# Performance work log

Measured on AMD Instinct MI355X. Metric: run time of the kernel, lower is better.

The kernel has to match this reference:

```python
import jax, jax.numpy as jnp
import numpy as np

N_EMBD = 512
N_HEAD = 8
HEAD = N_EMBD // N_HEAD
EPS = 1e-5

def layernorm(x, g, b):
    mu = jnp.mean(x, axis=-1, keepdims=True)
    var = jnp.mean(jnp.square(x - mu), axis=-1, keepdims=True)
    return (x - mu) * jax.lax.rsqrt(var + EPS) * g + b

def setup_inputs() -> dict:
    key = jax.random.key(0)
    ks = jax.random.split(key, 12)
    B, T, C, H, D = 32, 512, N_EMBD, N_HEAD, HEAD
    s = lambda fan: 1.0 / np.sqrt(fan)
    return {
        "x": jax.random.normal(ks[0], (B, T, C), jnp.float32),
        "wq": jax.random.normal(ks[1], (H, C, D), jnp.float32) * s(C),
        "wk": jax.random.normal(ks[2], (H, C, D), jnp.float32) * s(C),
        "wv": jax.random.normal(ks[3], (H, C, D), jnp.float32) * s(C),
        "w_proj": jax.random.normal(ks[4], (C, C), jnp.float32) * s(C),
        "b_proj": jnp.zeros((C,), jnp.float32),
        "w1": jax.random.normal(ks[5], (C, 4 * C), jnp.float32) * s(C),
        "b1": jnp.zeros((4 * C,), jnp.float32),
        "w2": jax.random.normal(ks[6], (4 * C, C), jnp.float32) * s(4 * C),
        "b2": jnp.zeros((C,), jnp.float32),
        "ln1_g": jnp.ones((C,), jnp.float32),
        "ln1_b": jnp.zeros((C,), jnp.float32),
        "ln2_g": jnp.ones((C,), jnp.float32),
        "ln2_b": jnp.zeros((C,), jnp.float32),
    }

def reference(x, wq, wk, wv, w_proj, b_proj, w1, b1, w2, b2, ln1_g, ln1_b, ln2_g, ln2_b):
    B, T, C = x.shape
    h = layernorm(x, ln1_g, ln1_b)
    q = jnp.einsum('btc,hcd->bhtd', h, wq)
    k = jnp.einsum('btc,hcd->bhtd', h, wk)
    v = jnp.einsum('btc,hcd->bhtd', h, wv)
    # NB: original scales by n_embd**-0.5 (C), not head_size
    scores = jnp.einsum('bhtd,bhsd->bhts', q, k) * (C ** -0.5)
    causal = jnp.tril(jnp.ones((T, T), bool))
    scores = jnp.where(causal, scores, -jnp.inf)
    attn = jax.nn.softmax(scores, axis=-1)
    o = jnp.einsum('bhts,bhsd->bhtd', attn, v)  # [B,H,T,D]
    o = jnp.transpose(o, (0, 2, 1, 3)).reshape(B, T, C)  # concat heads
    x = x + o @ w_proj + b_proj
    h2 = layernorm(x, ln2_g, ln2_b)
    ffn = jax.nn.relu(h2 @ w1 + b1) @ w2 + b2
    return x + ffn
```

## Files before the change

kernel.cpp:

```cpp
#include <hip/hip_runtime.h>
#include <hip/hip_bf16.h>


#define B_  32
#define T_  512
#define C_  512
#define H_  8
#define D_  64
#define BT  (B_*T_)
#define CF  2048

typedef __hip_bfloat16 bf16;
typedef __attribute__((ext_vector_type(8))) short bf16x8;
typedef __attribute__((ext_vector_type(4))) float f32x4;
typedef __attribute__((ext_vector_type(4))) short short4v;

__device__ __forceinline__ float bf2f(bf16 x) { return __bfloat162float(x); }
__device__ __forceinline__ bf16  f2bf(float x){ return __float2bfloat16(x); }
__device__ __forceinline__ short f2bf_bits(float f){
    bf16 h = __float2bfloat16(f);
    return *reinterpret_cast<short*>(&h);
}
__device__ __forceinline__ float bfbits2f(short s){
    unsigned u = ((unsigned)(unsigned short)s) << 16;
    return __uint_as_float(u);
}

#define AS_G __attribute__((address_space(1)))
#define AS_L __attribute__((address_space(3)))

__global__ __launch_bounds__(256) void transpose_all(const float* __restrict__ wq,
                                                     const float* __restrict__ wk,
                                                     const float* __restrict__ wv,
                                                     const float* __restrict__ wproj,
                                                     const float* __restrict__ w1,
                                                     const float* __restrict__ w2,
                                                     bf16* __restrict__ wt)
{
    const int t = blockIdx.x;
    const float* src; int K, Nn, k0, n0; size_t dstoff;
    if (t < 192) {
        const int which = t / 64, w = t % 64, hh = w >> 3, kt = w & 7;
        src = (which == 0 ? wq : which == 1 ? wk : wv) + (size_t)hh * 512 * 64;
        K = 512; Nn = 64; k0 = kt * 64; n0 = 0;
        dstoff = (size_t)(which * 512 + hh * 64) * 512;
    } else if (t < 256) {
        const int i = t - 192;
        src = wproj; K = 512; Nn = 512; n0 = (i & 7) * 64; k0 = (i >> 3) * 64;
        dstoff = (size_t)1536 * 512;
    } else if (t < 512) {
        const int i = t - 256;
        src = w1; K = 512; Nn = 2048; n0 = (i & 31) * 64; k0 = (i >> 5) * 64;
        dstoff = (size_t)2048 * 512;
    } else {
        const int i = t - 512;
        src = w2; K = 2048; Nn = 512; n0 = (i & 7) * 64; k0 = (i >> 3) * 64;
        dstoff = (size_t)2048 * 512 + (size_t)2048 * 512;
    }

    __shared__ float tl[64][65];
    const int tid = threadIdx.x;
    #pragma unroll
    for (int j = 0; j < 16; ++j) {
        const int e = j * 256 + tid, r = e >> 6, c = e & 63;
        tl[r][c] = src[(size_t)(k0 + r) * Nn + n0 + c];
    }
    __syncthreads();
    #pragma unroll
    for (int j = 0; j < 16; ++j) {
        const int e = j * 256 + tid, n = e >> 6, kk = e & 63;
        wt[dstoff + (size_t)(n0 + n) * K + k0 + kk] = f2bf(tl[kk][n]);
    }
}

__global__ __launch_bounds__(256) void ln_kernel(const float* __restrict__ x,
                                                 const float* __restrict__ g,
                                                 const float* __restrict__ b,
                                                 bf16* __restrict__ out)
{
    const int row = blockIdx.x;
    const int tid = threadIdx.x;
    const float* xr = x + (size_t)row * C_;
    float v0 = xr[tid], v1 = xr[tid + 256];

    __shared__ float red[4];

    float s = v0 + v1;
    #pragma unroll
    for (int off = 32; off > 0; off >>= 1) s += __shfl_down(s, off, 64);
    if ((tid & 63) == 0) red[tid >> 6] = s;
    __syncthreads();
    const float mean = (red[0] + red[1] + red[2] + red[3]) * (1.0f / C_);
    __syncthreads();

    float d0 = v0 - mean, d1 = v1 - mean;
    float vs = d0 * d0 + d1 * d1;
    #pragma unroll
    for (int off = 32; off > 0; off >>= 1) vs += __shfl_down(vs, off, 64);
    if ((tid & 63) == 0) red[tid >> 6] = vs;
    __syncthreads();
    const float var  = (red[0] + red[1] + red[2] + red[3]) * (1.0f / C_);
    const float rstd = rsqrtf(var + 1e-5f);

    bf16* orow = out + (size_t)row * C_;
    orow[tid]       = f2bf(d0 * rstd * g[tid]       + b[tid]);
    orow[tid + 256] = f2bf(d1 * rstd * g[tid + 256] + b[tid + 256]);
}

template<bool QKV, bool RELU, bool OUT_BF16>
__global__ __launch_bounds__(256, 2) void mfma_gemm(const bf16* __restrict__ A,
                                                    const bf16* __restrict__ Bt,
                                                    const float* __restrict__ bias,
                                                    const float* __restrict__ res,
                                                    void* __restrict__ outp,
                                                    int N, int K)
{
    __shared__ __align__(16) bf16 As[2][128 * 64];
    __shared__ __align__(16) bf16 Bs[2][128 * 64];

    const int tid  = threadIdx.x;
    const int wave = tid >> 6, lane = tid & 63;
    const int l16  = lane & 15, quad = lane >> 4;
    const int wm   = wave >> 1, wn = wave & 1;

    const int nwg = gridDim.x * gridDim.y;
    int bid = blockIdx.y * gridDim.x + blockIdx.x;
    bid = (bid & 7) * (nwg >> 3) + (bid >> 3);
    const int tn = (bid % gridDim.x) * 128;
    const int tm = (bid / gridDim.x) * 128;
    const bool vblk = QKV && (tn >= 1024);

    f32x4 acc[4][4];
    #pragma unroll
    for (int i = 0; i < 4; ++i)
        #pragma unroll
        for (int j = 0; j < 4; ++j) acc[i][j] = (f32x4){0.f, 0.f, 0.f, 0.f};

    auto STAGE = [&](int buf, int k0) {
        #pragma unroll
        for (int j = 0; j < 4; ++j) {
            const int g = j * 256 + tid;
            const int row = g >> 3, phys = g & 7;
            const int c = phys ^ (row & 7);
            __builtin_amdgcn_global_load_lds((const AS_G void*)(A  + (size_t)(tm + row) * K + k0 + c * 8),
                                             (AS_L void*)&As[buf][(size_t)g * 8], 16, 0, 0);
            __builtin_amdgcn_global_load_lds((const AS_G void*)(Bt + (size_t)(tn + row) * K + k0 + c * 8),
                                             (AS_L void*)&Bs[buf][(size_t)g * 8], 16, 0, 0);
        }
    };

    STAGE(0, 0);
    __syncthreads();

    int cur = 0;
    for (int k0 = 0; k0 < K; k0 += 64) {
        if (k0 + 64 < K) STAGE(cur ^ 1, k0 + 64);

        #pragma unroll
        for (int half = 0; half < 2; ++half) {
            bf16x8 af[4], bfr[4];
            #pragma unroll
            for (int mf = 0; mf < 4; ++mf) {
                const int r = wm * 64 + mf * 16 + l16;
                const int p = (half * 4 + quad) ^ (r & 7);
                af[mf] = *(const bf16x8*)&As[cur][r * 64 + p * 8];
            }
            #pragma unroll
            for (int nf = 0; nf < 4; ++nf) {
                const int r = wn * 64 + nf * 16 + l16;
                const int p = (half * 4 + quad) ^ (r & 7);
                bfr[nf] = *(const bf16x8*)&Bs[cur][r * 64 + p * 8];
            }
            if (vblk) {
                #pragma unroll
                for (int mf = 0; mf < 4; ++mf)
                    #pragma unroll
                    for (int nf = 0; nf < 4; ++nf)
                        acc[mf][nf] = __builtin_amdgcn_mfma_f32_16x16x32_bf16(af[mf], bfr[nf], acc[mf][nf], 0, 0, 0);
            } else {
                #pragma unroll
                for (int mf = 0; mf < 4; ++mf)
                    #pragma unroll
                    for (int nf = 0; nf < 4; ++nf)
                        acc[mf][nf] = __builtin_amdgcn_mfma_f32_16x16x32_bf16(bfr[nf], af[mf], acc[mf][nf], 0, 0, 0);
            }
        }

        __syncthreads();
        cur ^= 1;
    }

    if (QKV) {
        bf16* qkv = (bf16*)outp;
        if (!vblk) {
            const int which = tn >> 9;
            bf16* dst = qkv + (size_t)which * (8u << 20);
            #pragma unroll
            for (int mf = 0; mf < 4; ++mf) {
                const int m = tm + wm * 64 + mf * 16 + l16;
                const int bb = m >> 9, t = m & 511;
                #pragma unroll
                for (int nf = 0; nf < 4; ++nf) {
                    const int nb = tn + wn * 64 + nf * 16 + quad * 4;
                    const int hh = (nb >> 6) & 7, dd = nb & 63;
                    short4v pk;
                    #pragma unroll
                    for (int r = 0; r < 4; ++r) pk[r] = f2bf_bits(acc[mf][nf][r]);
                    *(short4v*)&dst[((size_t)(bb * 8 + hh) * 512 + t) * 64 + dd] = pk;
                }
            }
        } else {
            bf16* dst = qkv + (size_t)2 * (8u << 20);
            #pragma unroll
            for (int mf = 0; mf < 4; ++mf) {
                const int mb = tm + wm * 64 + mf * 16 + quad * 4;
                const int bb = mb >> 9, t = mb & 511;
                #pragma unroll
                for (int nf = 0; nf < 4; ++nf) {
                    const int n = tn + wn * 64 + nf * 16 + l16;
                    const int hh = (n >> 6) & 7, dd = n & 63;
                    short4v pk;
                    #pragma unroll
                    for (int r = 0; r < 4; ++r) pk[r] = f2bf_bits(acc[mf][nf][r]);
                    *(short4v*)&dst[((size_t)(bb * 8 + hh) * 64 + dd) * 512 + t] = pk;
                }
            }
        }
    } else {
        #pragma unroll
        for (int mf = 0; mf < 4; ++mf) {
            const int m = tm + wm * 64 + mf * 16 + l16;
            #pragma unroll
            for (int nf = 0; nf < 4; ++nf) {
                const int nb = tn + wn * 64 + nf * 16 + quad * 4;
                f32x4 a = acc[mf][nf];
                if (bias) a += *(const f32x4*)&bias[nb];
                if (RELU) {
                    #pragma unroll
                    for (int r = 0; r < 4; ++r) a[r] = fmaxf(a[r], 0.0f);
                }
                if (res)  a += *(const f32x4*)&res[(size_t)m * N + nb];
                if (OUT_BF16) {
                    short4v pk;
                    #pragma unroll
                    for (int r = 0; r < 4; ++r) pk[r] = f2bf_bits(a[r]);
                    *(short4v*)&((bf16*)outp)[(size_t)m * N + nb] = pk;
                } else {
                    *(f32x4*)&((float*)outp)[(size_t)m * N + nb] = a;
                }
            }
        }
    }
}


#define ATTN_TILE(qa, m_i, l_i, Of, qw, qtT)                                          \
  do {                                                                                \
    f32x4 Sf[4];                                                                      \
    _Pragma("unroll")                                                                 \
    for (int kf = 0; kf < 4; ++kf) {                                                  \
        const int row = kf * 16 + l16;                                                \
        bf16x8 b0 = *(const bf16x8*)&Ks[cur][row * 64 + ((quad ^ (row & 7)) * 8)];    \
        bf16x8 b1 = *(const bf16x8*)&Ks[cur][row * 64 + (((4 + quad) ^ (row & 7)) * 8)]; \
        f32x4 z = (f32x4){0.f, 0.f, 0.f, 0.f};                                        \
        z = __builtin_amdgcn_mfma_f32_16x16x32_bf16(qa[0], b0, z, 0, 0, 0);           \
        z = __builtin_amdgcn_mfma_f32_16x16x32_bf16(qa[1], b1, z, 0, 0, 0);           \
        Sf[kf] = z;                                                                   \
    }                                                                                 \
    if (kt == qtT) {                                                                  \
        _Pragma("unroll")                                                             \
        for (int kf = 0; kf < 4; ++kf)                                                \
            _Pragma("unroll")                                                         \
            for (int r = 0; r < 4; ++r)                                               \
                if (kt * 64 + kf * 16 + l16 > (qw) + quad * 4 + r) Sf[kf][r] = -1e30f;\
    }                                                                                 \
    float mnew[4], alpha[4];                                                          \
    _Pragma("unroll")                                                                 \
    for (int r = 0; r < 4; ++r) {                                                     \
        float v = fmaxf(fmaxf(Sf[0][r], Sf[1][r]), fmaxf(Sf[2][r], Sf[3][r]));        \
        v = fmaxf(v, __shfl_xor(v, 1, 64));                                           \
        v = fmaxf(v, __shfl_xor(v, 2, 64));                                           \
        v = fmaxf(v, __shfl_xor(v, 4, 64));                                           \
        v = fmaxf(v, __shfl_xor(v, 8, 64));                                           \
        mnew[r]   = fmaxf(m_i[r], v);                                                 \
        alpha[r]  = __expf(m_i[r] - mnew[r]);                                         \
        m_i[r]    = mnew[r];                                                          \
    }                                                                                 \
    float rs[4] = {0.f, 0.f, 0.f, 0.f};                                               \
    _Pragma("unroll")                                                                 \
    for (int kf = 0; kf < 4; ++kf) {                                                  \
        _Pragma("unroll")                                                             \
        for (int r = 0; r < 4; ++r) {                                                 \
            float p = __expf(Sf[kf][r] - mnew[r]);                                    \
            rs[r] += p;                                                               \
            Pw[wave][quad * 4 + r][kf * 16 + l16] = f2bf(p);                          \
        }                                                                             \
    }                                                                                 \
    _Pragma("unroll")                                                                 \
    for (int r = 0; r < 4; ++r) {                                                     \
        rs[r] += __shfl_xor(rs[r], 1, 64);                                            \
        rs[r] += __shfl_xor(rs[r], 2, 64);                                            \
        rs[r] += __shfl_xor(rs[r], 4, 64);                                            \
        rs[r] += __shfl_xor(rs[r], 8, 64);                                            \
        l_i[r] = l_i[r] * alpha[r] + rs[r];                                           \
    }                                                                                 \
    _Pragma("unroll")                                                                 \
    for (int f = 0; f < 4; ++f)                                                       \
        _Pragma("unroll")                                                             \
        for (int r = 0; r < 4; ++r)                                                   \
            Of[f][r] *= alpha[r];                                                     \
    bf16x8 pa0 = *(const bf16x8*)&Pw[wave][l16][quad * 8];                            \
    bf16x8 pa1 = *(const bf16x8*)&Pw[wave][l16][32 + quad * 8];                       \
    _Pragma("unroll")                                                                 \
    for (int f = 0; f < 4; ++f) {                                                     \
        const int vrow = f * 16 + l16;                                                \
        bf16x8 vb0 = *(const bf16x8*)&Vt[cur][vrow * 64 + ((quad ^ (vrow & 7)) * 8)]; \
        bf16x8 vb1 = *(const bf16x8*)&Vt[cur][vrow * 64 + (((4 + quad) ^ (vrow & 7)) * 8)]; \
        Of[f] = __builtin_amdgcn_mfma_f32_16x16x32_bf16(pa0, vb0, Of[f], 0, 0, 0);    \
        Of[f] = __builtin_amdgcn_mfma_f32_16x16x32_bf16(pa1, vb1, Of[f], 0, 0, 0);    \
    }                                                                                 \
  } while (0)

__global__ __launch_bounds__(256, 2) void attn_kernel(const bf16* __restrict__ q,
                                                      const bf16* __restrict__ kM,
                                                      const bf16* __restrict__ vT,
                                                      bf16* __restrict__ o)
{
    __shared__ __align__(16) bf16 Ks[2][64 * 64];
    __shared__ __align__(16) bf16 Vt[2][64 * 64];
    __shared__ __align__(16) bf16 Pw[4][16][72];

    const int tid  = threadIdx.x;
    const int wave = tid >> 6, lane = tid & 63;
    const int l16  = lane & 15, quad = lane >> 4;

    const int nwg = gridDim.x * gridDim.y;
    int bid = blockIdx.y * gridDim.x + blockIdx.x;
    bid = (bid & 7) * (nwg >> 3) + (bid >> 3);
    const int pair = bid & 3;
    const int bh   = bid >> 2;

    const int qt0 = pair, qt1 = 7 - pair;
    const int qw0 = qt0 * 64 + wave * 16;
    const int qw1 = qt1 * 64 + wave * 16;

    const float scale = 0.04419417382415922f;
    bf16x8 qa0[2], qa1[2];
    #pragma unroll
    for (int c = 0; c < 2; ++c) {
        bf16x8 t0 = *(const bf16x8*)(q + ((size_t)bh * T_ + qw0 + l16) * 64 + c * 32 + quad * 8);
        bf16x8 t1 = *(const bf16x8*)(q + ((size_t)bh * T_ + qw1 + l16) * 64 + c * 32 + quad * 8);
        #pragma unroll
        for (int j = 0; j < 8; ++j) {
            t0[j] = f2bf_bits(bfbits2f(t0[j]) * scale);
            t1[j] = f2bf_bits(bfbits2f(t1[j]) * scale);
        }
        qa0[c] = t0; qa1[c] = t1;
    }

    float m0[4], l0[4], m1[4], l1[4];
    f32x4 O0[4], O1[4];
    #pragma unroll
    for (int r = 0; r < 4; ++r) { m0[r] = -1e30f; l0[r] = 0.f; m1[r] = -1e30f; l1[r] = 0.f; }
    #pragma unroll
    for (int f = 0; f < 4; ++f) { O0[f] = (f32x4){0.f,0.f,0.f,0.f}; O1[f] = (f32x4){0.f,0.f,0.f,0.f}; }

    auto STAGE = [&](int buf, int kt) {
        const int k0 = kt * 64;
        #pragma unroll
        for (int j = 0; j < 2; ++j) {
            const int g = j * 256 + tid;
            const int row = g >> 3, phys = g & 7;
            const int c = phys ^ (row & 7);
            __builtin_amdgcn_global_load_lds((const AS_G void*)(kM + ((size_t)bh * T_ + k0 + row) * 64 + c * 8),
                                             (AS_L void*)&Ks[buf][(size_t)g * 8], 16, 0, 0);
            __builtin_amdgcn_global_load_lds((const AS_G void*)(vT + ((size_t)bh * 64 + row) * T_ + k0 + c * 8),
                                             (AS_L void*)&Vt[buf][(size_t)g * 8], 16, 0, 0);
        }
    };

    STAGE(0, 0);
    __syncthreads();

    int cur = 0;
    for (int kt = 0; kt <= qt1; ++kt) {
        if (kt < qt1) STAGE(cur ^ 1, kt + 1);

        if (kt <= qt0) ATTN_TILE(qa0, m0, l0, O0, qw0, qt0);
        ATTN_TILE(qa1, m1, l1, O1, qw1, qt1);

        __syncthreads();
        cur ^= 1;
    }

    const int b = bh >> 3, hh = bh & 7;
    #pragma unroll
    for (int r = 0; r < 4; ++r) {
        const float inv0 = 1.0f / l0[r];
        const float inv1 = 1.0f / l1[r];
        const int t0 = qw0 + quad * 4 + r;
        const int t1 = qw1 + quad * 4 + r;
        #pragma unroll
        for (int f = 0; f < 4; ++f) {
            o[((size_t)b * T_ + t0) * C_ + hh * 64 + f * 16 + l16] = f2bf(O0[f][r] * inv0);
            o[((size_t)b * T_ + t1) * C_ + hh * 64 + f * 16 + l16] = f2bf(O1[f][r] * inv1);
        }
    }
}

extern "C" void kernel_launch(void* const* d_in, const int* in_sizes, int n_in,
                              void* d_out, int out_size, void* d_ws, size_t ws_size,
                              hipStream_t stream)
{
    const float* x     = (const float*)d_in[0];
    const float* wq    = (const float*)d_in[1];
    const float* wk    = (const float*)d_in[2];
    const float* wv    = (const float*)d_in[3];
    const float* wproj = (const float*)d_in[4];
    const float* bproj = (const float*)d_in[5];
    const float* w1    = (const float*)d_in[6];
    const float* b1    = (const float*)d_in[7];
    const float* w2    = (const float*)d_in[8];
    const float* b2    = (const float*)d_in[9];
    const float* ln1g  = (const float*)d_in[10];
    const float* ln1b  = (const float*)d_in[11];
    const float* ln2g  = (const float*)d_in[12];
    const float* ln2b  = (const float*)d_in[13];

    char* ws = (char*)d_ws;
    bf16*  h    = (bf16*)(ws + 0);
    bf16*  q    = (bf16*)(ws + ((size_t)16 << 20));
    bf16*  k    = (bf16*)(ws + ((size_t)32 << 20));
    bf16*  v    = (bf16*)(ws + ((size_t)48 << 20));
    bf16*  mid  = (bf16*)(ws + 0);
    bf16*  o    = (bf16*)(ws + ((size_t)64 << 20));
    bf16*  h2   = (bf16*)(ws + ((size_t)80 << 20));
    bf16*  wt   = (bf16*)(ws + ((size_t)96 << 20));
    bf16*  projt = wt + (size_t)1536 * 512;
    bf16*  w1t   = wt + (size_t)2048 * 512;
    bf16*  w2t   = wt + (size_t)4096 * 512;
    float* x1    = (float*)d_out;

    transpose_all<<<768, 256, 0, stream>>>(wq, wk, wv, wproj, w1, w2, wt);

    ln_kernel<<<BT, 256, 0, stream>>>(x, ln1g, ln1b, h);

    mfma_gemm<true,  false, true ><<<dim3(12, 128), 256, 0, stream>>>(h, wt, nullptr, nullptr, q, 1536, 512);

    attn_kernel<<<dim3(4, B_ * H_), 256, 0, stream>>>(q, k, v, o);

    mfma_gemm<false, false, false><<<dim3(4, 128), 256, 0, stream>>>(o, projt, bproj, x, x1, 512, 512);

    ln_kernel<<<BT, 256, 0, stream>>>(x1, ln2g, ln2b, h2);

    mfma_gemm<false, true,  true ><<<dim3(16, 128), 256, 0, stream>>>(h2, w1t, b1, nullptr, mid, 2048, 512);

    mfma_gemm<false, false, false><<<dim3(4, 128), 256, 0, stream>>>(mid, w2t, b2, x1, (float*)d_out, 512, 2048);
}
```

Measured before the change: 335.6 us.

## Replace GEMM with 8-wave 256x128 tile and triple-buffered A pipeline

Replaces the 4-wave 128x128 double-buffered GEMM with a 512-thread kernel that computes a 256x128 tile. A is triple-buffered and B double-buffered in 128KB of dynamic LDS. Each K step is split into two half-M phases, with explicit vmcnt waits, raw barriers, sched barriers and s_setprio around the MFMA bursts, so global-to-LDS loads overlap compute. The aim is more reuse per loaded B tile and better hiding of memory latency. The cost is that the LDS footprint likely limits occupancy to one block per CU, and correctness now depends on the hand-counted load waits.

```diff
diff --git a/kernel.cpp b/kernel.cpp
--- a/kernel.cpp
+++ b/kernel.cpp
@@ -28,6 +28,8 @@
 
 #define AS_G __attribute__((address_space(1)))
 #define AS_L __attribute__((address_space(3)))
+
+#define SCHED_FENCE() __builtin_amdgcn_sched_barrier(0)
 
 __global__ __launch_bounds__(256) void transpose_all(const float* __restrict__ wq,
                                                      const float* __restrict__ wk,
@@ -108,86 +110,143 @@
 }
 
 template<bool QKV, bool RELU, bool OUT_BF16>
-__global__ __launch_bounds__(256, 2) void mfma_gemm(const bf16* __restrict__ A,
-                                                    const bf16* __restrict__ Bt,
-                                                    const float* __restrict__ bias,
-                                                    const float* __restrict__ res,
-                                                    void* __restrict__ outp,
-                                                    int N, int K)
+__global__ __launch_bounds__(512, 2) void gemm8(const bf16* __restrict__ A,
+                                                const bf16* __restrict__ Bt,
+                                                const float* __restrict__ bias,
+                                                const float* __restrict__ res,
+                                                void* __restrict__ outp,
+                                                int N, int K)
 {
-    __shared__ __align__(16) bf16 As[2][128 * 64];
-    __shared__ __align__(16) bf16 Bs[2][128 * 64];
+    extern __shared__ char smem[];
+    bf16* const Asl = (bf16*)smem;
+    bf16* const Bsl = (bf16*)(smem + 3 * 256 * 64 * 2);
 
     const int tid  = threadIdx.x;
-    const int wave = tid >> 6, lane = tid & 63;
+    const int lane = tid & 63, wid = tid >> 6;
     const int l16  = lane & 15, quad = lane >> 4;
-    const int wm   = wave >> 1, wn = wave & 1;
-
-    const int nwg = gridDim.x * gridDim.y;
-    int bid = blockIdx.y * gridDim.x + blockIdx.x;
+    const int wm   = wid >> 2, wn = wid & 3;
+
+    const int gridx = gridDim.x;
+    const int nwg = gridx * gridDim.y;
+    int bid = blockIdx.y * gridx + blockIdx.x;
     bid = (bid & 7) * (nwg >> 3) + (bid >> 3);
-    const int tn = (bid % gridDim.x) * 128;
-    const int tm = (bid / gridDim.x) * 128;
+    const int tn = (bid % gridx) * 128;
+    const int tm = (bid / gridx) * 256;
     const bool vblk = QKV && (tn >= 1024);
-
-    f32x4 acc[4][4];
-    #pragma unroll
-    for (int i = 0; i < 4; ++i)
-        #pragma unroll
-        for (int j = 0; j < 4; ++j) acc[i][j] = (f32x4){0.f, 0.f, 0.f, 0.f};
-
-    auto STAGE = [&](int buf, int k0) {
+    const int NT = K >> 6;
+
+    f32x4 acc[8][2];
+    #pragma unroll
+    for (int i = 0; i < 8; ++i)
+        #pragma unroll
+        for (int j = 0; j < 2; ++j) acc[i][j] = (f32x4){0.f, 0.f, 0.f, 0.f};
+
+    auto SA = [&](int s, int u) {
+        bf16* dst = Asl + s * (256 * 64);
+        const int k0 = u * 64;
         #pragma unroll
         for (int j = 0; j < 4; ++j) {
-            const int g = j * 256 + tid;
+            const int g = j * 512 + tid;
             const int row = g >> 3, phys = g & 7;
             const int c = phys ^ (row & 7);
-            __builtin_amdgcn_global_load_lds((const AS_G void*)(A  + (size_t)(tm + row) * K + k0 + c * 8),
-                                             (AS_L void*)&As[buf][(size_t)g * 8], 16, 0, 0);
+            __builtin_amdgcn_global_load_lds((const AS_G void*)(A + (size_t)(tm + row) * K + k0 + c * 8),
+                                             (AS_L void*)(dst + (size_t)g * 8), 16, 0, 0);
+        }
+    };
+    auto SB = [&](int s, int u) {
+        bf16* dst = Bsl + s * (128 * 64);
+        const int k0 = u * 64;
+        #pragma unroll
+        for (int j = 0; j < 2; ++j) {
+            const int g = j * 512 + tid;
+            const int row = g >> 3, phys = g & 7;
+            const int c = phys ^ (row & 7);
             __builtin_amdgcn_global_load_lds((const AS_G void*)(Bt + (size_t)(tn + row) * K + k0 + c * 8),
-                                             (AS_L void*)&Bs[buf][(size_t)g * 8], 16, 0, 0);
+                                             (AS_L void*)(dst + (size_t)g * 8), 16, 0, 0);
         }
     };
 
-    STAGE(0, 0);
-    __syncthreads();
-
-    int cur = 0;
-    for (int k0 = 0; k0 < K; k0 += 64) {
-        if (k0 + 64 < K) STAGE(cur ^ 1, k0 + 64);
-
-        #pragma unroll
-        for (int half = 0; half < 2; ++half) {
-            bf16x8 af[4], bfr[4];
-            #pragma unroll
-            for (int mf = 0; mf < 4; ++mf) {
-                const int r = wm * 64 + mf * 16 + l16;
-                const int p = (half * 4 + quad) ^ (r & 7);
-                af[mf] = *(const bf16x8*)&As[cur][r * 64 + p * 8];
+    SA(0, 0); SB(0, 0);
+    if (NT > 1) SA(1, 1);
+    asm volatile("s_waitcnt vmcnt(4)" ::: "memory");
+    SCHED_FENCE();
+    __builtin_amdgcn_s_barrier();
+    SCHED_FENCE();
+
+    int sa = 0;
+    for (int u = 0; u < NT; ++u) {
+        const bf16* Ab = Asl + sa * (256 * 64);
+        const bf16* Bb = Bsl + (u & 1) * (128 * 64);
+
+        bf16x8 bfr[2][2], af[4][2];
+        #pragma unroll
+        for (int nf = 0; nf < 2; ++nf)
+            #pragma unroll
+            for (int kh = 0; kh < 2; ++kh) {
+                const int r = wn * 32 + nf * 16 + l16;
+                const int p = (kh * 4 + quad) ^ (r & 7);
+                bfr[nf][kh] = *(const bf16x8*)&Bb[r * 64 + p * 8];
             }
-            #pragma unroll
-            for (int nf = 0; nf < 4; ++nf) {
-                const int r = wn * 64 + nf * 16 + l16;
-                const int p = (half * 4 + quad) ^ (r & 7);
-                bfr[nf] = *(const bf16x8*)&Bs[cur][r * 64 + p * 8];
+        #pragma unroll
+        for (int mf = 0; mf < 4; ++mf)
+            #pragma unroll
+            for (int kh = 0; kh < 2; ++kh) {
+                const int r = wm * 128 + mf * 16 + l16;
+                const int p = (kh * 4 + quad) ^ (r & 7);
+                af[mf][kh] = *(const bf16x8*)&Ab[r * 64 + p * 8];
             }
-            if (vblk) {
+        if (u + 1 < NT) SB((u + 1) & 1, u + 1);
+        SCHED_FENCE();
+        __builtin_amdgcn_s_barrier();
+        SCHED_FENCE();
+        __builtin_amdgcn_s_setprio(1);
+        #pragma unroll
+        for (int mf = 0; mf < 4; ++mf)
+            #pragma unroll
+            for (int nf = 0; nf < 2; ++nf)
                 #pragma unroll
-                for (int mf = 0; mf < 4; ++mf)
-                    #pragma unroll
-                    for (int nf = 0; nf < 4; ++nf)
-                        acc[mf][nf] = __builtin_amdgcn_mfma_f32_16x16x32_bf16(af[mf], bfr[nf], acc[mf][nf], 0, 0, 0);
-            } else {
+                for (int kh = 0; kh < 2; ++kh) {
+                    if (vblk) acc[mf][nf] = __builtin_amdgcn_mfma_f32_16x16x32_bf16(af[mf][kh], bfr[nf][kh], acc[mf][nf], 0, 0, 0);
+                    else      acc[mf][nf] = __builtin_amdgcn_mfma_f32_16x16x32_bf16(bfr[nf][kh], af[mf][kh], acc[mf][nf], 0, 0, 0);
+                }
+        __builtin_amdgcn_s_setprio(0);
+        SCHED_FENCE();
+        __builtin_amdgcn_s_barrier();
+        SCHED_FENCE();
+
+        #pragma unroll
+        for (int mf = 0; mf < 4; ++mf)
+            #pragma unroll
+            for (int kh = 0; kh < 2; ++kh) {
+                const int r = wm * 128 + 64 + mf * 16 + l16;
+                const int p = (kh * 4 + quad) ^ (r & 7);
+                af[mf][kh] = *(const bf16x8*)&Ab[r * 64 + p * 8];
+            }
+        if (u + 2 < NT) {
+            SA(sa == 0 ? 2 : sa - 1, u + 2);
+            asm volatile("s_waitcnt vmcnt(4)" ::: "memory");
+        } else {
+            asm volatile("s_waitcnt vmcnt(0)" ::: "memory");
+        }
+        SCHED_FENCE();
+        __builtin_amdgcn_s_barrier();
+        SCHED_FENCE();
+        __builtin_amdgcn_s_setprio(1);
+        #pragma unroll
+        for (int mf = 0; mf < 4; ++mf)
+            #pragma unroll
+            for (int nf = 0; nf < 2; ++nf)
                 #pragma unroll
-                for (int mf = 0; mf < 4; ++mf)
-                    #pragma unroll
-                    for (int nf = 0; nf < 4; ++nf)
-                        acc[mf][nf] = __builtin_amdgcn_mfma_f32_16x16x32_bf16(bfr[nf], af[mf], acc[mf][nf], 0, 0, 0);
-            }
-        }
-
-        __syncthreads();
-        cur ^= 1;
+                for (int kh = 0; kh < 2; ++kh) {
+                    if (vblk) acc[4 + mf][nf] = __builtin_amdgcn_mfma_f32_16x16x32_bf16(af[mf][kh], bfr[nf][kh], acc[4 + mf][nf], 0, 0, 0);
+                    else      acc[4 + mf][nf] = __builtin_amdgcn_mfma_f32_16x16x32_bf16(bfr[nf][kh], af[mf][kh], acc[4 + mf][nf], 0, 0, 0);
+                }
+        __builtin_amdgcn_s_setprio(0);
+        SCHED_FENCE();
+        __builtin_amdgcn_s_barrier();
+        SCHED_FENCE();
+
+        sa = (sa == 2) ? 0 : sa + 1;
     }
 
     if (QKV) {
@@ -196,12 +255,12 @@
             const int which = tn >> 9;
             bf16* dst = qkv + (size_t)which * (8u << 20);
             #pragma unroll
-            for (int mf = 0; mf < 4; ++mf) {
-                const int m = tm + wm * 64 + mf * 16 + l16;
+            for (int mf = 0; mf < 8; ++mf) {
+                const int m = tm + wm * 128 + mf * 16 + l16;
                 const int bb = m >> 9, t = m & 511;
                 #pragma unroll
-                for (int nf = 0; nf < 4; ++nf) {
-                    const int nb = tn + wn * 64 + nf * 16 + quad * 4;
+                for (int nf = 0; nf < 2; ++nf) {
+                    const int nb = tn + wn * 32 + nf * 16 + quad * 4;
                     const int hh = (nb >> 6) & 7, dd = nb & 63;
                     short4v pk;
                     #pragma unroll
@@ -212,12 +271,12 @@
         } else {
             bf16* dst = qkv + (size_t)2 * (8u << 20);
             #pragma unroll
-            for (int mf = 0; mf < 4; ++mf) {
-                const int mb = tm + wm * 64 + mf * 16 + quad * 4;
+            for (int mf = 0; mf < 8; ++mf) {
+                const int mb = tm + wm * 128 + mf * 16 + quad * 4;
                 const int bb = mb >> 9, t = mb & 511;
                 #pragma unroll
-                for (int nf = 0; nf < 4; ++nf) {
-                    const int n = tn + wn * 64 + nf * 16 + l16;
+                for (int nf = 0; nf < 2; ++nf) {
+                    const int n = tn + wn * 32 + nf * 16 + l16;
                     const int hh = (n >> 6) & 7, dd = n & 63;
                     short4v pk;
                     #pragma unroll
@@ -228,11 +287,11 @@
         }
     } else {
         #pragma unroll
-        for (int mf = 0; mf < 4; ++mf) {
-            const int m = tm + wm * 64 + mf * 16 + l16;
-            #pragma unroll
-            for (int nf = 0; nf < 4; ++nf) {
-                const int nb = tn + wn * 64 + nf * 16 + quad * 4;
+        for (int mf = 0; mf < 8; ++mf) {
+            const int m = tm + wm * 128 + mf * 16 + l16;
+            #pragma unroll
+            for (int nf = 0; nf < 2; ++nf) {
+                const int nb = tn + wn * 32 + nf * 16 + quad * 4;
                 f32x4 a = acc[mf][nf];
                 if (bias) a += *(const f32x4*)&bias[nb];
                 if (RELU) {
@@ -252,7 +311,6 @@
         }
     }
 }
-
 
 #define ATTN_TILE(qa, m_i, l_i, Of, qw, qtT)                                          \
   do {                                                                                \
@@ -441,19 +499,30 @@
     bf16*  w2t   = wt + (size_t)4096 * 512;
     float* x1    = (float*)d_out;
 
+    static bool smem_init = false;
+    if (!smem_init) {
+        smem_init = true;
+        hipFuncSetAttribute(reinterpret_cast<const void*>(&gemm8<true,  false, true >),
+                            hipFuncAttributeMaxDynamicSharedMemorySize, 131072);
+        hipFuncSetAttribute(reinterpret_cast<const void*>(&gemm8<false, false, false>),
+                            hipFuncAttributeMaxDynamicSharedMemorySize, 131072);
+        hipFuncSetAttribute(reinterpret_cast<const void*>(&gemm8<false, true,  true >),
+                            hipFuncAttributeMaxDynamicSharedMemorySize, 131072);
+    }
+
     transpose_all<<<768, 256, 0, stream>>>(wq, wk, wv, wproj, w1, w2, wt);
 
     ln_kernel<<<BT, 256, 0, stream>>>(x, ln1g, ln1b, h);
 
-    mfma_gemm<true,  false, true ><<<dim3(12, 128), 256, 0, stream>>>(h, wt, nullptr, nullptr, q, 1536, 512);
+    gemm8<true,  false, true ><<<dim3(12, 64), 512, 131072, stream>>>(h, wt, nullptr, nullptr, q, 1536, 512);
 
     attn_kernel<<<dim3(4, B_ * H_), 256, 0, stream>>>(q, k, v, o);
 
-    mfma_gemm<false, false, false><<<dim3(4, 128), 256, 0, stream>>>(o, projt, bproj, x, x1, 512, 512);
+    gemm8<false, false, false><<<dim3(4, 64), 512, 131072, stream>>>(o, projt, bproj, x, x1, 512, 512);
 
     ln_kernel<<<BT, 256, 0, stream>>>(x1, ln2g, ln2b, h2);
 
-    mfma_gemm<false, true,  true ><<<dim3(16, 128), 256, 0, stream>>>(h2, w1t, b1, nullptr, mid, 2048, 512);
-
-    mfma_gemm<false, false, false><<<dim3(4, 128), 256, 0, stream>>>(mid, w2t, b2, x1, (float*)d_out, 512, 2048);
-}
+    gemm8<false, true,  true ><<<dim3(16, 64), 512, 131072, stream>>>(h2, w1t, b1, nullptr, mid, 2048, 512);
+
+    gemm8<false, false, false><<<dim3(4, 64), 512, 131072, stream>>>(mid, w2t, b2, x1, (float*)d_out, 512, 2048);
+}
```

After: 358.1 us. 1.07x slower.

## Add 256x256-tile 8-phase pipelined GEMM for QKV and FFN-up projections

Applied to the files above, without the earlier changes.

Introduces a new GEMM kernel with 512 threads and 256x256 output tiles. It streams A and B into 128 KB of double-buffered LDS with global_load_lds and splits each K-pair iteration into eight barrier-gated phases that interleave LDS fragment loads, async global prefetch and MFMA bursts under raised wave priority. It also remaps block indices across XCD-sized groups. The QKV and FFN-up GEMMs switch to this kernel, while the old kernel keeps the proj and FFN-down GEMMs with its QKV epilogue removed. The larger tiles raise data reuse but need many accumulator registers and many barriers, which limits occupancy.

```diff
diff --git a/kernel.cpp b/kernel.cpp
--- a/kernel.cpp
+++ b/kernel.cpp
@@ -28,6 +28,8 @@
 
 #define AS_G __attribute__((address_space(1)))
 #define AS_L __attribute__((address_space(3)))
+
+#define SCHED_FENCE() __builtin_amdgcn_sched_barrier(0)
 
 __global__ __launch_bounds__(256) void transpose_all(const float* __restrict__ wq,
                                                      const float* __restrict__ wk,
@@ -190,43 +192,7 @@
         cur ^= 1;
     }
 
-    if (QKV) {
-        bf16* qkv = (bf16*)outp;
-        if (!vblk) {
-            const int which = tn >> 9;
-            bf16* dst = qkv + (size_t)which * (8u << 20);
-            #pragma unroll
-            for (int mf = 0; mf < 4; ++mf) {
-                const int m = tm + wm * 64 + mf * 16 + l16;
-                const int bb = m >> 9, t = m & 511;
-                #pragma unroll
-                for (int nf = 0; nf < 4; ++nf) {
-                    const int nb = tn + wn * 64 + nf * 16 + quad * 4;
-                    const int hh = (nb >> 6) & 7, dd = nb & 63;
-                    short4v pk;
-                    #pragma unroll
-                    for (int r = 0; r < 4; ++r) pk[r] = f2bf_bits(acc[mf][nf][r]);
-                    *(short4v*)&dst[((size_t)(bb * 8 + hh) * 512 + t) * 64 + dd] = pk;
-                }
-            }
-        } else {
-            bf16* dst = qkv + (size_t)2 * (8u << 20);
-            #pragma unroll
-            for (int mf = 0; mf < 4; ++mf) {
-                const int mb = tm + wm * 64 + mf * 16 + quad * 4;
-                const int bb = mb >> 9, t = mb & 511;
-                #pragma unroll
-                for (int nf = 0; nf < 4; ++nf) {
-                    const int n = tn + wn * 64 + nf * 16 + l16;
-                    const int hh = (n >> 6) & 7, dd = n & 63;
-                    short4v pk;
-                    #pragma unroll
-                    for (int r = 0; r < 4; ++r) pk[r] = f2bf_bits(acc[mf][nf][r]);
-                    *(short4v*)&dst[((size_t)(bb * 8 + hh) * 64 + dd) * 512 + t] = pk;
-                }
-            }
-        }
-    } else {
+    {
         #pragma unroll
         for (int mf = 0; mf < 4; ++mf) {
             const int m = tm + wm * 64 + mf * 16 + l16;
@@ -253,6 +219,223 @@
     }
 }
 
+template<bool QKV, bool RELU, bool OUT_BF16>
+__global__ __launch_bounds__(512, 2) void gemm8ph(const bf16* __restrict__ A,
+                                                  const bf16* __restrict__ Bt,
+                                                  const float* __restrict__ bias,
+                                                  const float* __restrict__ res,
+                                                  void* __restrict__ outp,
+                                                  int N, int K)
+{
+    extern __shared__ __align__(16) char smem[];
+    bf16* const As0 = (bf16*)smem;
+    bf16* const As1 = As0 + 256 * 64;
+    bf16* const Bs0 = As1 + 256 * 64;
+    bf16* const Bs1 = Bs0 + 256 * 64;
+
+    const int tid  = threadIdx.x;
+    const int lane = tid & 63, wid = tid >> 6;
+    const int l16  = lane & 15, quad = lane >> 4;
+    const int wm   = wid >> 2, wn = wid & 3;
+
+    const int gridx = gridDim.x;
+    const int nwg   = gridx * gridDim.y;
+    int bid = blockIdx.y * gridx + blockIdx.x;
+    bid = (bid & 7) * (nwg >> 3) + (bid >> 3);
+    const int tn = (bid % gridx) * 256;
+    const int tm = (bid / gridx) * 256;
+    const bool vblk = QKV && (tn >= 1024);
+    const int NT = K >> 6, NI = NT >> 1;
+
+    f32x4 acc[2][4][4];
+    #pragma unroll
+    for (int q = 0; q < 2; ++q)
+        #pragma unroll
+        for (int i = 0; i < 4; ++i)
+            #pragma unroll
+            for (int j = 0; j < 4; ++j) acc[q][i][j] = (f32x4){0.f, 0.f, 0.f, 0.f};
+
+    bf16x8 af[4][2], bfr[4][2];
+
+#define SA8(dst, u, h) do {                                                          \
+    const int _k0 = (u) << 6;                                                        \
+    _Pragma("unroll")                                                                \
+    for (int _j = 0; _j < 2; ++_j) {                                                 \
+        const int _g = (h) * 1024 + _j * 512 + tid;                                  \
+        const int _r = _g >> 3, _p = _g & 7;                                         \
+        const int _c = _p ^ (_r & 7);                                                \
+        __builtin_amdgcn_global_load_lds((const AS_G void*)(A + (size_t)(tm + _r) * K + _k0 + _c * 8), \
+                                         (AS_L void*)((dst) + _g * 8), 16, 0, 0);    \
+    } } while (0)
+
+#define SB8(dst, u, h) do {                                                          \
+    const int _k0 = (u) << 6;                                                        \
+    _Pragma("unroll")                                                                \
+    for (int _j = 0; _j < 2; ++_j) {                                                 \
+        const int _g = (h) * 1024 + _j * 512 + tid;                                  \
+        const int _r = _g >> 3, _p = _g & 7;                                         \
+        const int _c = _p ^ (_r & 7);                                                \
+        __builtin_amdgcn_global_load_lds((const AS_G void*)(Bt + (size_t)(tn + _r) * K + _k0 + _c * 8), \
+                                         (AS_L void*)((dst) + _g * 8), 16, 0, 0);    \
+    } } while (0)
+
+#define LDA8(Ab, qm) do {                                                            \
+    _Pragma("unroll")                                                                \
+    for (int _mf = 0; _mf < 4; ++_mf)                                                \
+        _Pragma("unroll")                                                            \
+        for (int _kh = 0; _kh < 2; ++_kh) {                                          \
+            const int _r = wm * 128 + (qm) * 64 + _mf * 16 + l16;                    \
+            const int _p = (_kh * 4 + quad) ^ (_r & 7);                              \
+            af[_mf][_kh] = *(const bf16x8*)&(Ab)[_r * 64 + _p * 8];                  \
+        } } while (0)
+
+#define LDB8(Bb, qn) do {                                                            \
+    _Pragma("unroll")                                                                \
+    for (int _c2 = 0; _c2 < 2; ++_c2)                                                \
+        _Pragma("unroll")                                                            \
+        for (int _kh = 0; _kh < 2; ++_kh) {                                          \
+            const int _nf = (qn) * 2 + _c2;                                          \
+            const int _r = wn * 64 + _nf * 16 + l16;                                 \
+            const int _p = (_kh * 4 + quad) ^ (_r & 7);                              \
+            bfr[_nf][_kh] = *(const bf16x8*)&(Bb)[_r * 64 + _p * 8];                 \
+        } } while (0)
+
+#define MM8(qm, qn) do {                                                             \
+    __builtin_amdgcn_s_setprio(1);                                                   \
+    _Pragma("unroll")                                                                \
+    for (int _mf = 0; _mf < 4; ++_mf)                                                \
+        _Pragma("unroll")                                                            \
+        for (int _c2 = 0; _c2 < 2; ++_c2) {                                          \
+            const int _nf = (qn) * 2 + _c2;                                          \
+            _Pragma("unroll")                                                        \
+            for (int _kh = 0; _kh < 2; ++_kh) {                                      \
+                if (vblk) acc[qm][_mf][_nf] = __builtin_amdgcn_mfma_f32_16x16x32_bf16(af[_mf][_kh], bfr[_nf][_kh], acc[qm][_mf][_nf], 0, 0, 0); \
+                else      acc[qm][_mf][_nf] = __builtin_amdgcn_mfma_f32_16x16x32_bf16(bfr[_nf][_kh], af[_mf][_kh], acc[qm][_mf][_nf], 0, 0, 0); \
+            }                                                                        \
+        }                                                                            \
+    __builtin_amdgcn_s_setprio(0);                                                   \
+    } while (0)
+
+#define GATE8() do { SCHED_FENCE(); __builtin_amdgcn_s_barrier();                    \
+    asm volatile("s_waitcnt lgkmcnt(0)" ::: "memory"); SCHED_FENCE(); } while (0)
+#define ENDP8() do { SCHED_FENCE(); __builtin_amdgcn_s_barrier(); SCHED_FENCE(); } while (0)
+
+    SA8(As0, 0, 0); SA8(As0, 0, 1);
+    SB8(Bs0, 0, 0); SB8(Bs0, 0, 1);
+    SB8(Bs1, 1, 0); SB8(Bs1, 1, 1);
+    asm volatile("s_waitcnt vmcnt(4)" ::: "memory");
+    SCHED_FENCE();
+    __builtin_amdgcn_s_barrier();
+    SCHED_FENCE();
+
+    for (int i = 0; i < NI; ++i) {
+        const int t1 = 2 * i + 1, t2 = 2 * i + 2, t3 = 2 * i + 3;
+        const bool p2 = t2 < NT, p3 = t3 < NT, lastI = (i == NI - 1);
+
+        LDA8(As0, 0); LDB8(Bs0, 0);
+        SA8(As1, t1, 0);
+        GATE8(); MM8(0, 0); ENDP8();
+        LDB8(Bs0, 1);
+        SA8(As1, t1, 1);
+        GATE8(); MM8(0, 1); ENDP8();
+        LDA8(As0, 1);
+        if (p2) SB8(Bs0, t2, 0);
+        GATE8(); MM8(1, 1); ENDP8();
+        if (p2) SA8(As0, t2, 0);
+        if (lastI) asm volatile("s_waitcnt vmcnt(0)" ::: "memory");
+        else       asm volatile("s_waitcnt vmcnt(4)" ::: "memory");
+        GATE8(); MM8(1, 0); ENDP8();
+        LDA8(As1, 0); LDB8(Bs1, 0);
+        if (p2) SA8(As0, t2, 1);
+        GATE8(); MM8(0, 0); ENDP8();
+        LDB8(Bs1, 1);
+        if (p2) SB8(Bs0, t2, 1);
+        GATE8(); MM8(0, 1); ENDP8();
+        LDA8(As1, 1);
+        if (p3) SB8(Bs1, t3, 0);
+        GATE8(); MM8(1, 1); ENDP8();
+        if (p3) SB8(Bs1, t3, 1);
+        if (lastI) asm volatile("s_waitcnt vmcnt(0)" ::: "memory");
+        else       asm volatile("s_waitcnt vmcnt(4)" ::: "memory");
+        GATE8(); MM8(1, 0); ENDP8();
+    }
+
+#undef SA8
+#undef SB8
+#undef LDA8
+#undef LDB8
+#undef MM8
+#undef GATE8
+#undef ENDP8
+
+    if (QKV) {
+        bf16* qkv = (bf16*)outp;
+        if (!vblk) {
+            const int which = tn >> 9;
+            bf16* dst = qkv + (size_t)which * (8u << 20);
+            #pragma unroll
+            for (int qm = 0; qm < 2; ++qm)
+                #pragma unroll
+                for (int mf = 0; mf < 4; ++mf) {
+                    const int m = tm + wm * 128 + qm * 64 + mf * 16 + l16;
+                    const int bb = m >> 9, t = m & 511;
+                    #pragma unroll
+                    for (int nf = 0; nf < 4; ++nf) {
+                        const int nb = tn + wn * 64 + nf * 16 + quad * 4;
+                        const int hh = (nb >> 6) & 7, dd = nb & 63;
+                        short4v pk;
+                        #pragma unroll
+                        for (int r = 0; r < 4; ++r) pk[r] = f2bf_bits(acc[qm][mf][nf][r]);
+                        *(short4v*)&dst[((size_t)(bb * 8 + hh) * 512 + t) * 64 + dd] = pk;
+                    }
+                }
+        } else {
+            bf16* dst = qkv + (size_t)2 * (8u << 20);
+            #pragma unroll
+            for (int qm = 0; qm < 2; ++qm)
+                #pragma unroll
+                for (int mf = 0; mf < 4; ++mf) {
+                    const int mb = tm + wm * 128 + qm * 64 + mf * 16 + quad * 4;
+                    const int bb = mb >> 9, t = mb & 511;
+                    #pragma unroll
+                    for (int nf = 0; nf < 4; ++nf) {
+                        const int n = tn + wn * 64 + nf * 16 + l16;
+                        const int hh = (n >> 6) & 7, dd = n & 63;
+                        short4v pk;
+                        #pragma unroll
+                        for (int r = 0; r < 4; ++r) pk[r] = f2bf_bits(acc[qm][mf][nf][r]);
+                        *(short4v*)&dst[((size_t)(bb * 8 + hh) * 64 + dd) * 512 + t] = pk;
+                    }
+                }
+        }
+    } else {
+        #pragma unroll
+        for (int qm = 0; qm < 2; ++qm)
+            #pragma unroll
+            for (int mf = 0; mf < 4; ++mf) {
+                const int m = tm + wm * 128 + qm * 64 + mf * 16 + l16;
+                #pragma unroll
+                for (int nf = 0; nf < 4; ++nf) {
+                    const int nb = tn + wn * 64 + nf * 16 + quad * 4;
+                    f32x4 a = acc[qm][mf][nf];
+                    if (bias) a += *(const f32x4*)&bias[nb];
+                    if (RELU) {
+                        #pragma unroll
+                        for (int r = 0; r < 4; ++r) a[r] = fmaxf(a[r], 0.0f);
+                    }
+                    if (res)  a += *(const f32x4*)&res[(size_t)m * N + nb];
+                    if (OUT_BF16) {
+                        short4v pk;
+                        #pragma unroll
+                        for (int r = 0; r < 4; ++r) pk[r] = f2bf_bits(a[r]);
+                        *(short4v*)&((bf16*)outp)[(size_t)m * N + nb] = pk;
+                    } else {
+                        *(f32x4*)&((float*)outp)[(size_t)m * N + nb] = a;
+                    }
+                }
+            }
+    }
+}
 
 #define ATTN_TILE(qa, m_i, l_i, Of, qw, qtT)                                          \
   do {                                                                                \
@@ -441,11 +624,20 @@
     bf16*  w2t   = wt + (size_t)4096 * 512;
     float* x1    = (float*)d_out;
 
+    static bool smem_init = false;
+    if (!smem_init) {
+        smem_init = true;
+        hipFuncSetAttribute(reinterpret_cast<const void*>(&gemm8ph<true,  false, true>),
+                            hipFuncAttributeMaxDynamicSharedMemorySize, 131072);
+        hipFuncSetAttribute(reinterpret_cast<const void*>(&gemm8ph<false, true,  true>),
+                            hipFuncAttributeMaxDynamicSharedMemorySize, 131072);
+    }
+
     transpose_all<<<768, 256, 0, stream>>>(wq, wk, wv, wproj, w1, w2, wt);
 
     ln_kernel<<<BT, 256, 0, stream>>>(x, ln1g, ln1b, h);
 
-    mfma_gemm<true,  false, true ><<<dim3(12, 128), 256, 0, stream>>>(h, wt, nullptr, nullptr, q, 1536, 512);
+    gemm8ph<true,  false, true><<<dim3(6, 64), 512, 131072, stream>>>(h, wt, nullptr, nullptr, q, 1536, 512);
 
     attn_kernel<<<dim3(4, B_ * H_), 256, 0, stream>>>(q, k, v, o);
 
@@ -453,7 +645,7 @@
 
     ln_kernel<<<BT, 256, 0, stream>>>(x1, ln2g, ln2b, h2);
 
-    mfma_gemm<false, true,  true ><<<dim3(16, 128), 256, 0, stream>>>(h2, w1t, b1, nullptr, mid, 2048, 512);
+    gemm8ph<false, true,  true><<<dim3(8, 64), 512, 131072, stream>>>(h2, w1t, b1, nullptr, mid, 2048, 512);
 
     mfma_gemm<false, false, false><<<dim3(4, 128), 256, 0, stream>>>(mid, w2t, b2, x1, (float*)d_out, 512, 2048);
 }
```

Measured after the change: 349.2 us. 4.0% more time.

## Make GEMM kernel persistent with cross-tile prefetch of next tile's first K-slice

Applied to the files above, without the earlier changes.

Converts the GEMM to a persistent-style launch of 512 blocks, each processing TPB output tiles in sequence. On the last K step of a tile it prefetches the next tile's first K slice, so the epilogue overlaps with the next load and launch/tail overhead is reduced. Tile assignment is strided by block count with the same XCD swizzle. This risks lower occupancy balance and extra register pressure from the inlined epilogue inside the K loop.

```diff
diff --git a/kernel.cpp b/kernel.cpp
--- a/kernel.cpp
+++ b/kernel.cpp
@@ -113,7 +113,7 @@
                                                     const float* __restrict__ bias,
                                                     const float* __restrict__ res,
                                                     void* __restrict__ outp,
-                                                    int N, int K)
+                                                    int N, int K, int TPB)
 {
     __shared__ __align__(16) bf16 As[2][128 * 64];
     __shared__ __align__(16) bf16 Bs[2][128 * 64];
@@ -123,12 +123,10 @@
     const int l16  = lane & 15, quad = lane >> 4;
     const int wm   = wave >> 1, wn = wave & 1;
 
-    const int nwg = gridDim.x * gridDim.y;
-    int bid = blockIdx.y * gridDim.x + blockIdx.x;
-    bid = (bid & 7) * (nwg >> 3) + (bid >> 3);
-    const int tn = (bid % gridDim.x) * 128;
-    const int tm = (bid / gridDim.x) * 128;
-    const bool vblk = QKV && (tn >= 1024);
+    const int nwg = gridDim.x;
+    const int bid = blockIdx.x;
+    const int sbid = (bid & 7) * (nwg >> 3) + (bid >> 3);
+    const int ntx = N >> 7;
 
     f32x4 acc[4][4];
     #pragma unroll
@@ -136,7 +134,7 @@
         #pragma unroll
         for (int j = 0; j < 4; ++j) acc[i][j] = (f32x4){0.f, 0.f, 0.f, 0.f};
 
-    auto STAGE = [&](int buf, int k0) {
+    auto STAGE = [&](int buf, int tm, int tn, int k0) {
         #pragma unroll
         for (int j = 0; j < 4; ++j) {
             const int g = j * 256 + tid;
@@ -149,110 +147,132 @@
         }
     };
 
-    STAGE(0, 0);
-    __syncthreads();
-
-    int cur = 0;
-    for (int k0 = 0; k0 < K; k0 += 64) {
-        if (k0 + 64 < K) STAGE(cur ^ 1, k0 + 64);
-
-        #pragma unroll
-        for (int half = 0; half < 2; ++half) {
-            bf16x8 af[4], bfr[4];
-            #pragma unroll
-            for (int mf = 0; mf < 4; ++mf) {
-                const int r = wm * 64 + mf * 16 + l16;
-                const int p = (half * 4 + quad) ^ (r & 7);
-                af[mf] = *(const bf16x8*)&As[cur][r * 64 + p * 8];
+    auto EPILOGUE = [&](int tm, int tn, bool vblk) {
+        if (QKV) {
+            bf16* qkv = (bf16*)outp;
+            if (!vblk) {
+                const int which = tn >> 9;
+                bf16* dst = qkv + (size_t)which * (8u << 20);
+                #pragma unroll
+                for (int mf = 0; mf < 4; ++mf) {
+                    const int m = tm + wm * 64 + mf * 16 + l16;
+                    const int bb = m >> 9, t = m & 511;
+                    #pragma unroll
+                    for (int nf = 0; nf < 4; ++nf) {
+                        const int nb = tn + wn * 64 + nf * 16 + quad * 4;
+                        const int hh = (nb >> 6) & 7, dd = nb & 63;
+                        short4v pk;
+                        #pragma unroll
+                        for (int r = 0; r < 4; ++r) pk[r] = f2bf_bits(acc[mf][nf][r]);
+                        *(short4v*)&dst[((size_t)(bb * 8 + hh) * 512 + t) * 64 + dd] = pk;
+                    }
+                }
+            } else {
+                bf16* dst = qkv + (size_t)2 * (8u << 20);
+                #pragma unroll
+                for (int mf = 0; mf < 4; ++mf) {
+                    const int mb = tm + wm * 64 + mf * 16 + quad * 4;
+                    const int bb = mb >> 9, t = mb & 511;
+                    #pragma unroll
+                    for (int nf = 0; nf < 4; ++nf) {
+                        const int n = tn + wn * 64 + nf * 16 + l16;
+                        const int hh = (n >> 6) & 7, dd = n & 63;
+                        short4v pk;
+                        #pragma unroll
+                        for (int r = 0; r < 4; ++r) pk[r] = f2bf_bits(acc[mf][nf][r]);
+                        *(short4v*)&dst[((size_t)(bb * 8 + hh) * 64 + dd) * 512 + t] = pk;
+                    }
+                }
             }
-            #pragma unroll
-            for (int nf = 0; nf < 4; ++nf) {
-                const int r = wn * 64 + nf * 16 + l16;
-                const int p = (half * 4 + quad) ^ (r & 7);
-                bfr[nf] = *(const bf16x8*)&Bs[cur][r * 64 + p * 8];
-            }
-            if (vblk) {
-                #pragma unroll
-                for (int mf = 0; mf < 4; ++mf)
-                    #pragma unroll
-                    for (int nf = 0; nf < 4; ++nf)
-                        acc[mf][nf] = __builtin_amdgcn_mfma_f32_16x16x32_bf16(af[mf], bfr[nf], acc[mf][nf], 0, 0, 0);
-            } else {
-                #pragma unroll
-                for (int mf = 0; mf < 4; ++mf)
-                    #pragma unroll
-                    for (int nf = 0; nf < 4; ++nf)
-                        acc[mf][nf] = __builtin_amdgcn_mfma_f32_16x16x32_bf16(bfr[nf], af[mf], acc[mf][nf], 0, 0, 0);
-            }
-        }
-
-        __syncthreads();
-        cur ^= 1;
-    }
-
-    if (QKV) {
-        bf16* qkv = (bf16*)outp;
-        if (!vblk) {
-            const int which = tn >> 9;
-            bf16* dst = qkv + (size_t)which * (8u << 20);
+        } else {
             #pragma unroll
             for (int mf = 0; mf < 4; ++mf) {
                 const int m = tm + wm * 64 + mf * 16 + l16;
-                const int bb = m >> 9, t = m & 511;
                 #pragma unroll
                 for (int nf = 0; nf < 4; ++nf) {
                     const int nb = tn + wn * 64 + nf * 16 + quad * 4;
-                    const int hh = (nb >> 6) & 7, dd = nb & 63;
-                    short4v pk;
-                    #pragma unroll
-                    for (int r = 0; r < 4; ++r) pk[r] = f2bf_bits(acc[mf][nf][r]);
-                    *(short4v*)&dst[((size_t)(bb * 8 + hh) * 512 + t) * 64 + dd] = pk;
+                    f32x4 a = acc[mf][nf];
+                    if (bias) a += *(const f32x4*)&bias[nb];
+                    if (RELU) {
+                        #pragma unroll
+                        for (int r = 0; r < 4; ++r) a[r] = fmaxf(a[r], 0.0f);
+                    }
+                    if (res)  a += *(const f32x4*)&res[(size_t)m * N + nb];
+                    if (OUT_BF16) {
+                        short4v pk;
+                        #pragma unroll
+                        for (int r = 0; r < 4; ++r) pk[r] = f2bf_bits(a[r]);
+                        *(short4v*)&((bf16*)outp)[(size_t)m * N + nb] = pk;
+                    } else {
+                        *(f32x4*)&((float*)outp)[(size_t)m * N + nb] = a;
+                    }
                 }
             }
-        } else {
-            bf16* dst = qkv + (size_t)2 * (8u << 20);
+        }
+        #pragma unroll
+        for (int i = 0; i < 4; ++i)
             #pragma unroll
-            for (int mf = 0; mf < 4; ++mf) {
-                const int mb = tm + wm * 64 + mf * 16 + quad * 4;
-                const int bb = mb >> 9, t = mb & 511;
+            for (int j = 0; j < 4; ++j) acc[i][j] = (f32x4){0.f, 0.f, 0.f, 0.f};
+    };
+
+    {
+        const int t0 = sbid;
+        STAGE(0, (t0 / ntx) << 7, (t0 % ntx) << 7, 0);
+    }
+    __syncthreads();
+
+    int cur = 0;
+    for (int s = 0; s < TPB; ++s) {
+        const int tile = sbid + s * nwg;
+        const int tm = (tile / ntx) << 7, tn = (tile % ntx) << 7;
+        const bool vblk = QKV && (tn >= 1024);
+
+        for (int k0 = 0; k0 < K; k0 += 64) {
+            const bool lastk = (k0 + 64 >= K);
+            if (!lastk) {
+                STAGE(cur ^ 1, tm, tn, k0 + 64);
+            } else if (s + 1 < TPB) {
+                const int nt = sbid + (s + 1) * nwg;
+                STAGE(cur ^ 1, (nt / ntx) << 7, (nt % ntx) << 7, 0);
+            }
+
+            #pragma unroll
+            for (int half = 0; half < 2; ++half) {
+                bf16x8 af[4], bfr[4];
+                #pragma unroll
+                for (int mf = 0; mf < 4; ++mf) {
+                    const int r = wm * 64 + mf * 16 + l16;
+                    const int p = (half * 4 + quad) ^ (r & 7);
+                    af[mf] = *(const bf16x8*)&As[cur][r * 64 + p * 8];
+                }
                 #pragma unroll
                 for (int nf = 0; nf < 4; ++nf) {
-                    const int n = tn + wn * 64 + nf * 16 + l16;
-                    const int hh = (n >> 6) & 7, dd = n & 63;
-                    short4v pk;
+                    const int r = wn * 64 + nf * 16 + l16;
+                    const int p = (half * 4 + quad) ^ (r & 7);
+                    bfr[nf] = *(const bf16x8*)&Bs[cur][r * 64 + p * 8];
+                }
+                if (vblk) {
                     #pragma unroll
-                    for (int r = 0; r < 4; ++r) pk[r] = f2bf_bits(acc[mf][nf][r]);
-                    *(short4v*)&dst[((size_t)(bb * 8 + hh) * 64 + dd) * 512 + t] = pk;
+                    for (int mf = 0; mf < 4; ++mf)
+                        #pragma unroll
+                        for (int nf = 0; nf < 4; ++nf)
+                            acc[mf][nf] = __builtin_amdgcn_mfma_f32_16x16x32_bf16(af[mf], bfr[nf], acc[mf][nf], 0, 0, 0);
+                } else {
+                    #pragma unroll
+                    for (int mf = 0; mf < 4; ++mf)
+                        #pragma unroll
+                        for (int nf = 0; nf < 4; ++nf)
+                            acc[mf][nf] = __builtin_amdgcn_mfma_f32_16x16x32_bf16(bfr[nf], af[mf], acc[mf][nf], 0, 0, 0);
                 }
             }
-        }
-    } else {
-        #pragma unroll
-        for (int mf = 0; mf < 4; ++mf) {
-            const int m = tm + wm * 64 + mf * 16 + l16;
-            #pragma unroll
-            for (int nf = 0; nf < 4; ++nf) {
-                const int nb = tn + wn * 64 + nf * 16 + quad * 4;
-                f32x4 a = acc[mf][nf];
-                if (bias) a += *(const f32x4*)&bias[nb];
-                if (RELU) {
-                    #pragma unroll
-                    for (int r = 0; r < 4; ++r) a[r] = fmaxf(a[r], 0.0f);
-                }
-                if (res)  a += *(const f32x4*)&res[(size_t)m * N + nb];
-                if (OUT_BF16) {
-                    short4v pk;
-                    #pragma unroll
-                    for (int r = 0; r < 4; ++r) pk[r] = f2bf_bits(a[r]);
-                    *(short4v*)&((bf16*)outp)[(size_t)m * N + nb] = pk;
-                } else {
-                    *(f32x4*)&((float*)outp)[(size_t)m * N + nb] = a;
-                }
-            }
-        }
-    }
-}
-
+
+            if (lastk) EPILOGUE(tm, tn, vblk);
+
+            __syncthreads();
+            cur ^= 1;
+        }
+    }
+}
 
 #define ATTN_TILE(qa, m_i, l_i, Of, qw, qtT)                                          \
   do {                                                                                \
@@ -445,15 +465,15 @@
 
     ln_kernel<<<BT, 256, 0, stream>>>(x, ln1g, ln1b, h);
 
-    mfma_gemm<true,  false, true ><<<dim3(12, 128), 256, 0, stream>>>(h, wt, nullptr, nullptr, q, 1536, 512);
+    mfma_gemm<true,  false, true ><<<512, 256, 0, stream>>>(h, wt, nullptr, nullptr, q, 1536, 512, 3);
 
     attn_kernel<<<dim3(4, B_ * H_), 256, 0, stream>>>(q, k, v, o);
 
-    mfma_gemm<false, false, false><<<dim3(4, 128), 256, 0, stream>>>(o, projt, bproj, x, x1, 512, 512);
+    mfma_gemm<false, false, false><<<512, 256, 0, stream>>>(o, projt, bproj, x, x1, 512, 512, 1);
 
     ln_kernel<<<BT, 256, 0, stream>>>(x1, ln2g, ln2b, h2);
 
-    mfma_gemm<false, true,  true ><<<dim3(16, 128), 256, 0, stream>>>(h2, w1t, b1, nullptr, mid, 2048, 512);
-
-    mfma_gemm<false, false, false><<<dim3(4, 128), 256, 0, stream>>>(mid, w2t, b2, x1, (float*)d_out, 512, 2048);
-}
+    mfma_gemm<false, true,  true ><<<512, 256, 0, stream>>>(h2, w1t, b1, nullptr, mid, 2048, 512, 4);
+
+    mfma_gemm<false, false, false><<<512, 256, 0, stream>>>(mid, w2t, b2, x1, (float*)d_out, 512, 2048, 1);
+}
```

Result: slower. 360.1 us (+7.3%).
